# Performance work log

Hardware: AMD Instinct MI355X
Metric: run time of the kernel (lower is better)

Reference implementation:

```python
import jax, jax.numpy as jnp
import numpy as np

S, N, D = 8, 2048, 256

def setup_inputs() -> dict:
    key = jax.random.key(0)
    k0, k1, k2 = jax.random.split(key, 3)
    tensor0 = jax.random.normal(k0, (S, N, D), dtype=jnp.float32)
    tensor1 = jax.random.normal(k1, (S, N, D), dtype=jnp.float32)
    # glorot-ish scale for the (D, D) bilinear kernel
    kernel = jax.random.normal(k2, (D, D), dtype=jnp.float32) * (1.0 / np.sqrt(D))
    bias = jnp.zeros((1,), dtype=jnp.float32)  # scalar bias, shape () in keras
    return {"tensor0": tensor0, "tensor1": tensor1, "kernel": kernel, "bias": bias}

def reference(tensor0, tensor1, kernel, bias):
    # Faithful math of Bilinear(bilin_axes=[1]) on inputs [S, N, D]:
    # out[s, i, j] = sum_{d,e} tensor1[s,i,d] * kernel[d,e] * tensor0[s,j,e] + bias
    # (the original builds the full [S,N,S,N] cross tensor and extracts the
    #  batch diagonal; this einsum is the equivalent O(S*N*N*D) contraction).
    qt0 = jnp.einsum('de,sje->sjd', kernel, tensor0)      # [S, N, D]
    out = jnp.einsum('sid,sjd->sij', tensor1, qt0)        # [S, N, N]
    return out + bias[0]
```

## Files before the change

### kernel.cpp

```cpp
#include <hip/hip_runtime.h>
#include <hip/hip_bf16.h>


typedef __bf16 bf16x8 __attribute__((ext_vector_type(8)));
typedef float f32x4 __attribute__((ext_vector_type(4)));

__device__ __forceinline__ unsigned short f2bf(float f) {
  union { __hip_bfloat16 h; unsigned short u; } v;
  v.h = __float2bfloat16(f);
  return v.u;
}

__device__ __forceinline__ void cvt8_store(unsigned short* dst, const float* src) {
  float4 v0 = *(const float4*)src;
  float4 v1 = *(const float4*)(src + 4);
  union { unsigned short u[8]; uint4 q; } p;
  p.u[0] = f2bf(v0.x); p.u[1] = f2bf(v0.y); p.u[2] = f2bf(v0.z); p.u[3] = f2bf(v0.w);
  p.u[4] = f2bf(v1.x); p.u[5] = f2bf(v1.y); p.u[6] = f2bf(v1.z); p.u[7] = f2bf(v1.w);
  *(uint4*)dst = p.q;
}

__global__ __launch_bounds__(256, 2) void prep(
    const float* __restrict__ t0, const float4* __restrict__ t1,
    const float* __restrict__ kk, ushort4* __restrict__ T1b,
    unsigned short* __restrict__ Qb) {
  const int tid = threadIdx.x;

  if (blockIdx.x >= 256) {
    const int i0 = (blockIdx.x - 256) * 256 + tid;
#pragma unroll
    for (int it = 0; it < 4; it++) {
      const int j = i0 + it * 262144;
      float4 v = t1[j];
      T1b[j] = make_ushort4(f2bf(v.x), f2bf(v.y), f2bf(v.z), f2bf(v.w));
    }
    return;
  }

  __shared__ unsigned short sA[2][128 * 64];
  __shared__ unsigned short sB[2][128 * 64];

  const int wave = tid >> 6;
  const int lane = tid & 63;
  const int quad = lane >> 4;
  const int l16 = lane & 15;
  const int wrow = (wave >> 1) * 64;
  const int wcol = (wave & 1) * 64;
  const int rsw = (l16 & 7) * 8;

  const int brow = (blockIdx.x >> 1) * 128;
  const int bcol = (blockIdx.x & 1) * 128;

  const float* Af = t0 + (long long)brow * 256;
  const float* Bf = kk + (long long)bcol * 256;

  const int srow = lane >> 3;
  const int scol = ((lane & 7) ^ srow) * 8;

  auto stage1 = [&](unsigned short* dA, unsigned short* dB, int kt) {
#pragma unroll
    for (int i = 0; i < 4; i++) {
      const int rr = i * 32 + wave * 8 + srow;
      cvt8_store(dA + rr * 64 + (lane & 7) * 8,
                 Af + (long long)rr * 256 + kt + scol);
      cvt8_store(dB + rr * 64 + (lane & 7) * 8,
                 Bf + (long long)rr * 256 + kt + scol);
    }
  };

  f32x4 acc[4][4];
#pragma unroll
  for (int i = 0; i < 4; i++)
#pragma unroll
    for (int j = 0; j < 4; j++) acc[i][j] = (f32x4){0.f, 0.f, 0.f, 0.f};

  stage1(sA[0], sB[0], 0);

  int cur = 0;
  for (int kt = 0; kt < 256; kt += 64) {
    __syncthreads();
    const unsigned short* a = sA[cur];
    const unsigned short* b = sB[cur];
    bf16x8 af[4], bfr[4];
#pragma unroll
    for (int mi = 0; mi < 4; mi++)
      af[mi] = *(const bf16x8*)&a[(wrow + mi * 16 + l16) * 64 + ((quad * 8) ^ rsw)];
#pragma unroll
    for (int ni = 0; ni < 4; ni++)
      bfr[ni] = *(const bf16x8*)&b[(wcol + ni * 16 + l16) * 64 + ((quad * 8) ^ rsw)];
    if (kt + 64 < 256) stage1(sA[cur ^ 1], sB[cur ^ 1], kt + 64);
#pragma unroll
    for (int mi = 0; mi < 4; mi++)
#pragma unroll
      for (int ni = 0; ni < 4; ni++)
        acc[mi][ni] = __builtin_amdgcn_mfma_f32_16x16x32_bf16(
            af[mi], bfr[ni], acc[mi][ni], 0, 0, 0);
#pragma unroll
    for (int mi = 0; mi < 4; mi++)
      af[mi] = *(const bf16x8*)&a[(wrow + mi * 16 + l16) * 64 + ((32 + quad * 8) ^ rsw)];
#pragma unroll
    for (int ni = 0; ni < 4; ni++)
      bfr[ni] = *(const bf16x8*)&b[(wcol + ni * 16 + l16) * 64 + ((32 + quad * 8) ^ rsw)];
#pragma unroll
    for (int mi = 0; mi < 4; mi++)
#pragma unroll
      for (int ni = 0; ni < 4; ni++)
        acc[mi][ni] = __builtin_amdgcn_mfma_f32_16x16x32_bf16(
            af[mi], bfr[ni], acc[mi][ni], 0, 0, 0);
    cur ^= 1;
  }

#pragma unroll
  for (int mi = 0; mi < 4; mi++)
#pragma unroll
    for (int ni = 0; ni < 4; ni++) {
      const int r0 = brow + wrow + mi * 16 + quad * 4;
      const int c = bcol + wcol + ni * 16 + l16;
#pragma unroll
      for (int r = 0; r < 4; r++)
        Qb[(long long)(r0 + r) * 256 + c] = f2bf(acc[mi][ni][r]);
    }
}

template <bool OUT_BF16>
__global__ __launch_bounds__(256, 2) void gemm_nt(
    const unsigned short* __restrict__ A, const unsigned short* __restrict__ B,
    void* __restrict__ Cout, const float* __restrict__ bias,
    const int K, const int ldc,
    const long long aStride, const long long bStride, const long long cStride) {
  __shared__ unsigned short sA[2][128 * 64];
  __shared__ unsigned short sB[2][128 * 64];

  const int tid = threadIdx.x;
  const int wave = tid >> 6;
  const int lane = tid & 63;
  const int quad = lane >> 4;
  const int l16 = lane & 15;
  const int wrow = (wave >> 1) * 64;
  const int wcol = (wave & 1) * 64;
  const int rsw = (l16 & 7) * 8;

  const int brow = blockIdx.y * 128;
  const int bcol = blockIdx.x * 128;
  const long long bz = blockIdx.z;

  const unsigned short* Ab = A + bz * aStride + (long long)brow * K;
  const unsigned short* Bb = B + bz * bStride + (long long)bcol * K;

  const int srow = lane >> 3;
  const int scol = ((lane & 7) ^ srow) * 8;

  auto stage = [&](unsigned short* dA, unsigned short* dB, int kt) {
#pragma unroll
    for (int i = 0; i < 4; i++) {
      const int r = i * 32 + wave * 8;
      const unsigned short* ga = Ab + (long long)(r + srow) * K + kt + scol;
      const unsigned short* gb = Bb + (long long)(r + srow) * K + kt + scol;
      __builtin_amdgcn_global_load_lds(
          (const __attribute__((address_space(1))) unsigned int*)ga,
          (__attribute__((address_space(3))) unsigned int*)(dA + r * 64),
          16, 0, 0);
      __builtin_amdgcn_global_load_lds(
          (const __attribute__((address_space(1))) unsigned int*)gb,
          (__attribute__((address_space(3))) unsigned int*)(dB + r * 64),
          16, 0, 0);
    }
  };

  f32x4 acc[4][4];
#pragma unroll
  for (int i = 0; i < 4; i++)
#pragma unroll
    for (int j = 0; j < 4; j++) acc[i][j] = (f32x4){0.f, 0.f, 0.f, 0.f};

  stage(sA[0], sB[0], 0);

  int cur = 0;
  for (int kt = 0; kt < K; kt += 64) {
    __syncthreads();
    const unsigned short* a = sA[cur];
    const unsigned short* b = sB[cur];
    {
      bf16x8 af[4], bfr[4];
#pragma unroll
      for (int mi = 0; mi < 4; mi++)
        af[mi] = *(const bf16x8*)&a[(wrow + mi * 16 + l16) * 64 + ((quad * 8) ^ rsw)];
#pragma unroll
      for (int ni = 0; ni < 4; ni++)
        bfr[ni] = *(const bf16x8*)&b[(wcol + ni * 16 + l16) * 64 + ((quad * 8) ^ rsw)];
      if (kt + 64 < K) stage(sA[cur ^ 1], sB[cur ^ 1], kt + 64);
#pragma unroll
      for (int mi = 0; mi < 4; mi++)
#pragma unroll
        for (int ni = 0; ni < 4; ni++)
          acc[mi][ni] = __builtin_amdgcn_mfma_f32_16x16x32_bf16(
              af[mi], bfr[ni], acc[mi][ni], 0, 0, 0);
    }
    {
      bf16x8 af[4], bfr[4];
#pragma unroll
      for (int mi = 0; mi < 4; mi++)
        af[mi] = *(const bf16x8*)&a[(wrow + mi * 16 + l16) * 64 + ((32 + quad * 8) ^ rsw)];
#pragma unroll
      for (int ni = 0; ni < 4; ni++)
        bfr[ni] = *(const bf16x8*)&b[(wcol + ni * 16 + l16) * 64 + ((32 + quad * 8) ^ rsw)];
#pragma unroll
      for (int mi = 0; mi < 4; mi++)
#pragma unroll
        for (int ni = 0; ni < 4; ni++)
          acc[mi][ni] = __builtin_amdgcn_mfma_f32_16x16x32_bf16(
              af[mi], bfr[ni], acc[mi][ni], 0, 0, 0);
    }
    cur ^= 1;
  }

  if constexpr (OUT_BF16) {
    unsigned short* C = (unsigned short*)Cout + bz * cStride;
#pragma unroll
    for (int mi = 0; mi < 4; mi++)
#pragma unroll
      for (int ni = 0; ni < 4; ni++) {
        const int r0 = brow + wrow + mi * 16 + quad * 4;
        const int c = bcol + wcol + ni * 16 + l16;
#pragma unroll
        for (int r = 0; r < 4; r++)
          C[(long long)(r0 + r) * ldc + c] = f2bf(acc[mi][ni][r]);
      }
  } else {
    const float bv = bias[0];
    float* C = (float*)Cout + bz * cStride;
#pragma unroll
    for (int mi = 0; mi < 4; mi++)
#pragma unroll
      for (int ni = 0; ni < 4; ni++) {
        const int r0 = brow + wrow + mi * 16 + quad * 4;
        const int c = bcol + wcol + ni * 16 + l16;
#pragma unroll
        for (int r = 0; r < 4; r++)
          C[(long long)(r0 + r) * ldc + c] = acc[mi][ni][r] + bv;
      }
  }
}

extern "C" void kernel_launch(void* const* d_in, const int* in_sizes, int n_in,
                              void* d_out, int out_size, void* d_ws, size_t ws_size,
                              hipStream_t stream) {
  const float* t0 = (const float*)d_in[0];
  const float* t1 = (const float*)d_in[1];
  const float* kk = (const float*)d_in[2];
  const float* bias = (const float*)d_in[3];

  unsigned short* T1b = (unsigned short*)d_ws;
  unsigned short* Qb = T1b + 4194304;

  prep<<<1280, 256, 0, stream>>>(t0, (const float4*)t1, kk, (ushort4*)T1b, Qb);

  gemm_nt<false><<<dim3(16, 16, 8), 256, 0, stream>>>(
      T1b, Qb, d_out, bias, 256, 2048, 524288LL, 524288LL, 4194304LL);
}
```

Baseline: 180.3 us.

## Rewrite batched GEMM with 4-stage K=32 LDS pipeline and explicit vmcnt waits

Replaces the templated double-buffered GEMM (K tile 64) with a specialized kernel that uses a 4-deep ring of K=32 LDS buffers, prefetching three stages ahead and fully unrolling the 8 K-steps. Each step waits with an explicit s_waitcnt vmcnt and a raw barrier, and raises wave priority around the MFMA block. It also flattens the grid to 1D with the batch index innermost and hardcodes the shapes. The LDS XOR swizzle is dropped, which may add bank conflicts on the fragment reads, in exchange for hiding more global-load latency.

```diff
diff --git a/kernel.cpp b/kernel.cpp
--- a/kernel.cpp
+++ b/kernel.cpp
@@ -122,14 +122,11 @@
     }
 }
 
-template <bool OUT_BF16>
-__global__ __launch_bounds__(256, 2) void gemm_nt(
+__global__ __launch_bounds__(256, 2) void gemm2(
     const unsigned short* __restrict__ A, const unsigned short* __restrict__ B,
-    void* __restrict__ Cout, const float* __restrict__ bias,
-    const int K, const int ldc,
-    const long long aStride, const long long bStride, const long long cStride) {
-  __shared__ unsigned short sA[2][128 * 64];
-  __shared__ unsigned short sB[2][128 * 64];
+    float* __restrict__ Cout, const float* __restrict__ bias) {
+  __shared__ unsigned short sA[4][128 * 32];
+  __shared__ unsigned short sB[4][128 * 32];
 
   const int tid = threadIdx.x;
   const int wave = tid >> 6;
@@ -138,31 +135,31 @@
   const int l16 = lane & 15;
   const int wrow = (wave >> 1) * 64;
   const int wcol = (wave & 1) * 64;
-  const int rsw = (l16 & 7) * 8;
-
-  const int brow = blockIdx.y * 128;
-  const int bcol = blockIdx.x * 128;
-  const long long bz = blockIdx.z;
-
-  const unsigned short* Ab = A + bz * aStride + (long long)brow * K;
-  const unsigned short* Bb = B + bz * bStride + (long long)bcol * K;
-
-  const int srow = lane >> 3;
-  const int scol = ((lane & 7) ^ srow) * 8;
+
+  const int bid = blockIdx.x;
+  const long long s = bid & 7;
+  const int t = bid >> 3;
+  const int bcol = (t & 15) * 128;
+  const int brow = (t >> 4) * 128;
+
+  const unsigned short* Ab = A + s * 524288 + (long long)brow * 256;
+  const unsigned short* Bb = B + s * 524288 + (long long)bcol * 256;
+
+  const int srow = wave * 16 + (lane >> 2);
+  const int scol = (lane & 3) * 8;
 
   auto stage = [&](unsigned short* dA, unsigned short* dB, int kt) {
 #pragma unroll
-    for (int i = 0; i < 4; i++) {
-      const int r = i * 32 + wave * 8;
-      const unsigned short* ga = Ab + (long long)(r + srow) * K + kt + scol;
-      const unsigned short* gb = Bb + (long long)(r + srow) * K + kt + scol;
+    for (int half = 0; half < 2; half++) {
+      const unsigned short* ga = Ab + (long long)(half * 64 + srow) * 256 + kt + scol;
+      const unsigned short* gb = Bb + (long long)(half * 64 + srow) * 256 + kt + scol;
       __builtin_amdgcn_global_load_lds(
           (const __attribute__((address_space(1))) unsigned int*)ga,
-          (__attribute__((address_space(3))) unsigned int*)(dA + r * 64),
+          (__attribute__((address_space(3))) unsigned int*)(dA + (half * 64 + wave * 16) * 32),
           16, 0, 0);
       __builtin_amdgcn_global_load_lds(
           (const __attribute__((address_space(1))) unsigned int*)gb,
-          (__attribute__((address_space(3))) unsigned int*)(dB + r * 64),
+          (__attribute__((address_space(3))) unsigned int*)(dB + (half * 64 + wave * 16) * 32),
           16, 0, 0);
     }
   };
@@ -174,72 +171,49 @@
     for (int j = 0; j < 4; j++) acc[i][j] = (f32x4){0.f, 0.f, 0.f, 0.f};
 
   stage(sA[0], sB[0], 0);
-
-  int cur = 0;
-  for (int kt = 0; kt < K; kt += 64) {
-    __syncthreads();
-    const unsigned short* a = sA[cur];
-    const unsigned short* b = sB[cur];
-    {
-      bf16x8 af[4], bfr[4];
-#pragma unroll
-      for (int mi = 0; mi < 4; mi++)
-        af[mi] = *(const bf16x8*)&a[(wrow + mi * 16 + l16) * 64 + ((quad * 8) ^ rsw)];
-#pragma unroll
-      for (int ni = 0; ni < 4; ni++)
-        bfr[ni] = *(const bf16x8*)&b[(wcol + ni * 16 + l16) * 64 + ((quad * 8) ^ rsw)];
-      if (kt + 64 < K) stage(sA[cur ^ 1], sB[cur ^ 1], kt + 64);
-#pragma unroll
-      for (int mi = 0; mi < 4; mi++)
-#pragma unroll
-        for (int ni = 0; ni < 4; ni++)
-          acc[mi][ni] = __builtin_amdgcn_mfma_f32_16x16x32_bf16(
-              af[mi], bfr[ni], acc[mi][ni], 0, 0, 0);
-    }
-    {
-      bf16x8 af[4], bfr[4];
-#pragma unroll
-      for (int mi = 0; mi < 4; mi++)
-        af[mi] = *(const bf16x8*)&a[(wrow + mi * 16 + l16) * 64 + ((32 + quad * 8) ^ rsw)];
-#pragma unroll
-      for (int ni = 0; ni < 4; ni++)
-        bfr[ni] = *(const bf16x8*)&b[(wcol + ni * 16 + l16) * 64 + ((32 + quad * 8) ^ rsw)];
-#pragma unroll
-      for (int mi = 0; mi < 4; mi++)
-#pragma unroll
-        for (int ni = 0; ni < 4; ni++)
-          acc[mi][ni] = __builtin_amdgcn_mfma_f32_16x16x32_bf16(
-              af[mi], bfr[ni], acc[mi][ni], 0, 0, 0);
-    }
-    cur ^= 1;
+  stage(sA[1], sB[1], 32);
+  stage(sA[2], sB[2], 64);
+
+#define STEP(I, VM)                                                          \
+  {                                                                          \
+    asm volatile("s_waitcnt vmcnt(" #VM ")" ::: "memory");                   \
+    __builtin_amdgcn_s_barrier();                                            \
+    const unsigned short* a = sA[(I) & 3];                                   \
+    const unsigned short* b = sB[(I) & 3];                                   \
+    bf16x8 af[4], bfr[4];                                                    \
+    _Pragma("unroll")                                                        \
+    for (int mi = 0; mi < 4; mi++)                                           \
+      af[mi] = *(const bf16x8*)&a[(wrow + mi * 16 + l16) * 32 + quad * 8];   \
+    _Pragma("unroll")                                                        \
+    for (int ni = 0; ni < 4; ni++)                                           \
+      bfr[ni] = *(const bf16x8*)&b[(wcol + ni * 16 + l16) * 32 + quad * 8];  \
+    if ((I) < 5) stage(sA[((I) + 3) & 3], sB[((I) + 3) & 3], ((I) + 3) * 32);\
+    __builtin_amdgcn_s_setprio(1);                                           \
+    _Pragma("unroll")                                                        \
+    for (int mi = 0; mi < 4; mi++)                                           \
+      _Pragma("unroll")                                                      \
+      for (int ni = 0; ni < 4; ni++)                                         \
+        acc[mi][ni] = __builtin_amdgcn_mfma_f32_16x16x32_bf16(               \
+            af[mi], bfr[ni], acc[mi][ni], 0, 0, 0);                          \
+    __builtin_amdgcn_s_setprio(0);                                           \
   }
 
-  if constexpr (OUT_BF16) {
-    unsigned short* C = (unsigned short*)Cout + bz * cStride;
-#pragma unroll
-    for (int mi = 0; mi < 4; mi++)
-#pragma unroll
-      for (int ni = 0; ni < 4; ni++) {
-        const int r0 = brow + wrow + mi * 16 + quad * 4;
-        const int c = bcol + wcol + ni * 16 + l16;
-#pragma unroll
-        for (int r = 0; r < 4; r++)
-          C[(long long)(r0 + r) * ldc + c] = f2bf(acc[mi][ni][r]);
-      }
-  } else {
-    const float bv = bias[0];
-    float* C = (float*)Cout + bz * cStride;
-#pragma unroll
-    for (int mi = 0; mi < 4; mi++)
-#pragma unroll
-      for (int ni = 0; ni < 4; ni++) {
-        const int r0 = brow + wrow + mi * 16 + quad * 4;
-        const int c = bcol + wcol + ni * 16 + l16;
-#pragma unroll
-        for (int r = 0; r < 4; r++)
-          C[(long long)(r0 + r) * ldc + c] = acc[mi][ni][r] + bv;
-      }
-  }
+  STEP(0, 8) STEP(1, 8) STEP(2, 8) STEP(3, 8)
+  STEP(4, 8) STEP(5, 8) STEP(6, 4) STEP(7, 0)
+#undef STEP
+
+  const float bv = bias[0];
+  float* C = Cout + s * 4194304;
+#pragma unroll
+  for (int mi = 0; mi < 4; mi++)
+#pragma unroll
+    for (int ni = 0; ni < 4; ni++) {
+      const int r0 = brow + wrow + mi * 16 + quad * 4;
+      const int c = bcol + wcol + ni * 16 + l16;
+#pragma unroll
+      for (int r = 0; r < 4; r++)
+        C[(long long)(r0 + r) * 2048 + c] = acc[mi][ni][r] + bv;
+    }
 }
 
 extern "C" void kernel_launch(void* const* d_in, const int* in_sizes, int n_in,
@@ -255,6 +229,5 @@
 
   prep<<<1280, 256, 0, stream>>>(t0, (const float4*)t1, kk, (ushort4*)T1b, Qb);
 
-  gemm_nt<false><<<dim3(16, 16, 8), 256, 0, stream>>>(
-      T1b, Qb, d_out, bias, 256, 2048, 524288LL, 524288LL, 4194304LL);
-}
+  gemm2<<<2048, 256, 0, stream>>>(T1b, Qb, (float*)d_out, bias);
+}
```

New measurement: 180.2 us. No clear change (-0.0%).
